# Kernel optimization log

Measured on AMD Instinct MI355X. Metric: run time of the kernel, lower is better.

## Reference

```python
import jax, jax.numpy as jnp
import numpy as np

B, S = 4, 1024          # 4 prefill sequences of length 1024 (cu_seqlens equal-length)
D_MODEL = 2048
N_HEADS = 32
N_KV_HEADS = 8
HEAD_DIM = D_MODEL // N_HEADS          # 64
GROUPS = N_HEADS // N_KV_HEADS         # 4
ROPE_THETA = 10000.0
SCALE = HEAD_DIM ** -0.5


def setup_inputs() -> dict:
    key = jax.random.key(0)
    ks = jax.random.split(key, 6)
    T = B * S
    hidden_states = jax.random.normal(ks[0], (T, D_MODEL), jnp.float32)
    # rotary tables: positions restart per sequence (prefill)
    pos = jnp.tile(jnp.arange(S, dtype=jnp.float32), B)            # [T]
    inv_freq = 1.0 / (ROPE_THETA ** (jnp.arange(0, HEAD_DIM, 2, dtype=jnp.float32) / HEAD_DIM))
    freqs = pos[:, None] * inv_freq[None, :]                        # [T, HEAD_DIM/2]
    cos, sin = jnp.cos(freqs), jnp.sin(freqs)
    std = D_MODEL ** -0.5
    Wq = jax.random.normal(ks[1], (D_MODEL, N_HEADS * HEAD_DIM), jnp.float32) * std
    Wk = jax.random.normal(ks[2], (D_MODEL, N_KV_HEADS * HEAD_DIM), jnp.float32) * std
    Wv = jax.random.normal(ks[3], (D_MODEL, N_KV_HEADS * HEAD_DIM), jnp.float32) * std
    Wo = jax.random.normal(ks[4], (N_HEADS * HEAD_DIM, D_MODEL), jnp.float32) * std
    return {"hidden_states": hidden_states, "cos": cos, "sin": sin,
            "Wq": Wq, "Wk": Wk, "Wv": Wv, "Wo": Wo}


def _rope(x, cos, sin):
    # NeoX-style rotary: x [T, H, D], cos/sin [T, D/2]
    half = x.shape[-1] // 2
    x1, x2 = x[..., :half], x[..., half:]
    c, s = cos[:, None, :], sin[:, None, :]
    return jnp.concatenate([x1 * c - x2 * s, x2 * c + x1 * s], axis=-1)


def reference(hidden_states, cos, sin, Wq, Wk, Wv, Wo):
    T = hidden_states.shape[0]
    q = (hidden_states @ Wq).reshape(T, N_HEADS, HEAD_DIM)
    k = (hidden_states @ Wk).reshape(T, N_KV_HEADS, HEAD_DIM)
    v = (hidden_states @ Wv).reshape(T, N_KV_HEADS, HEAD_DIM)
    q = _rope(q, cos, sin)
    k = _rope(k, cos, sin)
    # equal-length varlen prefill -> [B, S, H, D]
    q = q.reshape(B, S, N_HEADS, HEAD_DIM)
    k = jnp.repeat(k.reshape(B, S, N_KV_HEADS, HEAD_DIM), GROUPS, axis=2)  # GQA expand
    v = jnp.repeat(v.reshape(B, S, N_KV_HEADS, HEAD_DIM), GROUPS, axis=2)
    scores = jnp.einsum("bqhd,bkhd->bhqk", q, k) * SCALE
    causal = jnp.tril(jnp.ones((S, S), dtype=bool))
    scores = jnp.where(causal[None, None], scores, jnp.finfo(scores.dtype).min)
    probs = jax.nn.softmax(scores, axis=-1)
    attn = jnp.einsum("bhqk,bkhd->bqhd", probs, v).reshape(T, N_HEADS * HEAD_DIM)
    return attn @ Wo
```

## Files before the change

### kernel.cpp

```cpp
#include <hip/hip_runtime.h>
#include <type_traits>


typedef __bf16 bf16x8 __attribute__((ext_vector_type(8)));
typedef __bf16 bf16x4 __attribute__((ext_vector_type(4)));
typedef float f32x4 __attribute__((ext_vector_type(4)));
typedef unsigned short u16;
typedef unsigned int u32;

#define DEVI __device__ __forceinline__

DEVI u16 f2bf(float f) {
  u32 u = __builtin_bit_cast(u32, f);
  u += 0x7FFF + ((u >> 16) & 1);
  return (u16)(u >> 16);
}

DEVI void ld16_lds(const void* g, void* l) {
  __builtin_amdgcn_global_load_lds((const __attribute__((address_space(1))) u32*)g,
                                   (__attribute__((address_space(3))) u32*)l, 16, 0, 0);
}

__global__ __launch_bounds__(256) void convert_f32_bf16(const float* __restrict__ src,
                                                        u16* __restrict__ dst, int n4) {
  int i = blockIdx.x * 256 + threadIdx.x;
  if (i >= n4) return;
  float4 v = ((const float4*)src)[i];
  ushort4 o;
  o.x = f2bf(v.x); o.y = f2bf(v.y); o.z = f2bf(v.z); o.w = f2bf(v.w);
  ((ushort4*)dst)[i] = o;
}

__global__ __launch_bounds__(256) void trans_f32_bf16(const float* __restrict__ src,
                                                      u16* __restrict__ dst, int R, int C,
                                                      float scale) {
  __shared__ float tile[32][33];
  int c0 = blockIdx.x * 32, r0 = blockIdx.y * 32;
  int tx = threadIdx.x & 31, ty = threadIdx.x >> 5;
#pragma unroll
  for (int i = 0; i < 32; i += 8)
    tile[ty + i][tx] = src[(size_t)(r0 + ty + i) * C + (c0 + tx)];
  __syncthreads();
#pragma unroll
  for (int i = 0; i < 32; i += 8)
    dst[(size_t)(c0 + ty + i) * R + (r0 + tx)] = f2bf(tile[tx][ty + i] * scale);
}

template <typename OutT, bool ROPE>
__global__ __launch_bounds__(256) void gemm_bt(const u16* __restrict__ A, const u16* __restrict__ BT,
                                               OutT* __restrict__ C, int M, int N, int K,
                                               const float* __restrict__ cs,
                                               const float* __restrict__ sn) {
  __shared__ u16 As[128 * 64];
  __shared__ u16 Bs[128 * 64];
  const int tid = threadIdx.x;
  const int lane = tid & 63, wave = tid >> 6;
  const int quad = lane >> 4, l16 = lane & 15;
  const int m0 = blockIdx.y * 128, n0 = blockIdx.x * 128;
  const int wr = (wave >> 1) * 64, wc = (wave & 1) * 64;

  f32x4 acc[4][4] = {};

  const int srow = tid >> 3;
  const int sc = (tid & 7) ^ (srow & 7);
  const u16* Ag = A + (size_t)(m0 + srow) * K + sc * 8;
  const u16* Bg = BT + (size_t)(n0 + srow) * K + sc * 8;

  for (int k0 = 0; k0 < K; k0 += 64) {
    __syncthreads();
#pragma unroll
    for (int i = 0; i < 4; i++) {
      ld16_lds(Ag + k0 + (size_t)i * 32 * K, &As[tid * 8 + i * 2048]);
      ld16_lds(Bg + k0 + (size_t)i * 32 * K, &Bs[tid * 8 + i * 2048]);
    }
    __syncthreads();

#pragma unroll
    for (int s = 0; s < 2; s++) {
      bf16x8 af[4], bfr[4];
#pragma unroll
      for (int i = 0; i < 4; i++) {
        int ar = wr + i * 16 + l16;
        af[i] = *(const bf16x8*)&As[ar * 64 + (((s * 4 + quad) ^ (ar & 7)) * 8)];
        int br = wc + i * 16 + l16;
        bfr[i] = *(const bf16x8*)&Bs[br * 64 + (((s * 4 + quad) ^ (br & 7)) * 8)];
      }
#pragma unroll
      for (int i = 0; i < 4; i++)
#pragma unroll
        for (int j = 0; j < 4; j++)
          acc[i][j] = __builtin_amdgcn_mfma_f32_16x16x32_bf16(af[i], bfr[j], acc[i][j], 0, 0, 0);
    }
  }

  if constexpr (ROPE) {
    if (n0 + wc < 2560) {
#pragma unroll
      for (int i = 0; i < 4; i++) {
        int t0 = m0 + wr + i * 16 + quad * 4;
#pragma unroll
        for (int jj = 0; jj < 2; jj++) {
          int d = jj * 16 + l16;
#pragma unroll
          for (int r = 0; r < 4; r++) {
            float c = cs[(size_t)(t0 + r) * 32 + d];
            float s = sn[(size_t)(t0 + r) * 32 + d];
            float x1 = acc[i][jj][r], x2 = acc[i][jj + 2][r];
            acc[i][jj][r] = x1 * c - x2 * s;
            acc[i][jj + 2][r] = x2 * c + x1 * s;
          }
        }
      }
    }
  }

#pragma unroll
  for (int i = 0; i < 4; i++) {
    int row = m0 + wr + i * 16 + quad * 4;
#pragma unroll
    for (int j = 0; j < 4; j++) {
      int col = n0 + wc + j * 16 + l16;
#pragma unroll
      for (int r = 0; r < 4; r++) {
        size_t off = (size_t)(row + r) * N + col;
        if constexpr (sizeof(OutT) == 2) C[off] = f2bf(acc[i][j][r]);
        else C[off] = acc[i][j][r];
      }
    }
  }
}

__global__ __launch_bounds__(256) void vkt_build(const u16* __restrict__ qkv,
                                                 u16* __restrict__ vkt) {
  __shared__ u16 Vn[128 * 64];
  const int kt = blockIdx.x, kvh = blockIdx.y, b = blockIdx.z;
  const int tid = threadIdx.x;
  const u16* src = qkv + ((size_t)b * 1024 + kt * 128) * 3072 + 2560 + kvh * 64;
  {
    int tok = tid >> 1, hf = tid & 1;
    const uint4* s4 = (const uint4*)(src + (size_t)tok * 3072 + hf * 32);
    uint4* d4 = (uint4*)&Vn[tok * 64 + hf * 32];
#pragma unroll
    for (int j = 0; j < 4; j++) d4[j] = s4[j];
  }
  __syncthreads();
  u16* img = vkt + ((((size_t)b * 8 + kvh) * 8 + kt) << 13);
#pragma unroll
  for (int i = 0; i < 4; i++) {
    int c = tid * 4 + i;
    int dd = c >> 4, chsw = c & 15;
    int ch = chsw ^ (dd & 15);
    u16 tmp[8];
#pragma unroll
    for (int p = 0; p < 8; p++) {
      int col = ch * 8 + p;
      int g = col >> 5, kl = col & 31;
      int kph = ((kl >> 2) & 1) * 16 + ((kl >> 4) & 1) * 8 + ((kl >> 3) & 1) * 4 + (kl & 3);
      tmp[p] = Vn[(g * 32 + kph) * 64 + dd];
    }
    *(uint4*)&img[c * 8] = *(const uint4*)tmp;
  }
}

__global__ __launch_bounds__(256, 2) void flash_attn(const u16* __restrict__ qkv,
                                                     const u16* __restrict__ vkt,
                                                     u16* __restrict__ attn) {
  __shared__ u16 Ks[2][128 * 64];
  __shared__ u16 VT[2][64 * 128];

  const int tid = threadIdx.x;
  const int lane = tid & 63, wave = tid >> 6;
  const int quad = lane >> 4, l16 = lane & 15;
  const int qtA = blockIdx.x, qtB = 7 - blockIdx.x;
  const int h = blockIdx.y, b = blockIdx.z, kvh = h >> 2;
  const size_t tokBase = (size_t)b * 1024;
  const int qcol = h * 64, kcol = 2048 + kvh * 64;
  const int srow = tid >> 3, spc = tid & 7, ssc = spc ^ (srow & 7);

  auto stageK = [&](const u16* gbase, u16* L) {
#pragma unroll
    for (int i = 0; i < 4; i++)
      ld16_lds(gbase + (size_t)(srow + i * 32) * 3072 + ssc * 8, &L[tid * 8 + i * 2048]);
  };
  const u16* vimg = vkt + (((size_t)b * 8 + kvh) << 16);
  auto stageV = [&](int kt, u16* L) {
    const u16* g = vimg + ((size_t)kt << 13);
#pragma unroll
    for (int i = 0; i < 4; i++)
      ld16_lds(g + i * 2048 + tid * 8, &L[tid * 8 + i * 2048]);
  };

  stageK(qkv + (tokBase + qtA * 128) * 3072 + qcol, Ks[0]);
  stageK(qkv + (tokBase + qtB * 128) * 3072 + qcol, Ks[1]);
  __syncthreads();
  bf16x8 qfA[2][2], qfB[2][2];
#pragma unroll
  for (int nq = 0; nq < 2; nq++) {
    int qrow = wave * 32 + nq * 16 + l16;
#pragma unroll
    for (int ks = 0; ks < 2; ks++) {
      int c = (ks * 4 + quad) ^ (qrow & 7);
      qfA[nq][ks] = *(const bf16x8*)&Ks[0][qrow * 64 + c * 8];
      qfB[nq][ks] = *(const bf16x8*)&Ks[1][qrow * 64 + c * 8];
    }
  }
  __syncthreads();

  float lA[2] = {0.f, 0.f}, lB[2] = {0.f, 0.f};
  f32x4 oA[4][2] = {}, oB[4][2] = {};

  auto proc = [&](const bf16x8 (&kf)[2][2], const bf16x8 (&va)[4], const bf16x8 (&qf)[2][2],
                  f32x4 (&o)[4][2], float (&lacc)[2], bool msk, int c) {
    f32x4 s[2][2] = {};
#pragma unroll
    for (int mkl = 0; mkl < 2; mkl++)
#pragma unroll
      for (int ks = 0; ks < 2; ks++) {
        s[0][mkl] = __builtin_amdgcn_mfma_f32_16x16x32_bf16(kf[mkl][ks], qf[0][ks], s[0][mkl], 0, 0, 0);
        s[1][mkl] = __builtin_amdgcn_mfma_f32_16x16x32_bf16(kf[mkl][ks], qf[1][ks], s[1][mkl], 0, 0, 0);
      }
    if (msk) {
#pragma unroll
      for (int nq = 0; nq < 2; nq++) {
        int q = wave * 32 + nq * 16 + l16;
#pragma unroll
        for (int mkl = 0; mkl < 2; mkl++)
#pragma unroll
          for (int r = 0; r < 4; r++)
            if ((c * 2 + mkl) * 16 + quad * 4 + r > q) s[nq][mkl][r] = -3e38f;
      }
    }
    bf16x8 pf[2];
#pragma unroll
    for (int nq = 0; nq < 2; nq++) {
      float a0 = 0.f;
#pragma unroll
      for (int mkl = 0; mkl < 2; mkl++)
#pragma unroll
        for (int r = 0; r < 4; r++) {
          float p = __builtin_amdgcn_exp2f(s[nq][mkl][r]);
          s[nq][mkl][r] = p;
          a0 += p;
        }
      lacc[nq] += a0;
      pf[nq][0] = (__bf16)s[nq][0][0]; pf[nq][1] = (__bf16)s[nq][0][1];
      pf[nq][2] = (__bf16)s[nq][0][2]; pf[nq][3] = (__bf16)s[nq][0][3];
      pf[nq][4] = (__bf16)s[nq][1][0]; pf[nq][5] = (__bf16)s[nq][1][1];
      pf[nq][6] = (__bf16)s[nq][1][2]; pf[nq][7] = (__bf16)s[nq][1][3];
    }
#pragma unroll
    for (int md = 0; md < 4; md++) {
      o[md][0] = __builtin_amdgcn_mfma_f32_16x16x32_bf16(va[md], pf[0], o[md][0], 0, 0, 0);
      o[md][1] = __builtin_amdgcn_mfma_f32_16x16x32_bf16(va[md], pf[1], o[md][1], 0, 0, 0);
    }
  };

  stageK(qkv + tokBase * 3072 + kcol, Ks[0]);
  stageV(0, VT[0]);

  for (int kt = 0; kt <= qtB; kt++) {
    const int cur = kt & 1;
    __syncthreads();
    if (kt < qtB) {
      stageK(qkv + (tokBase + (kt + 1) * 128) * 3072 + kcol, Ks[1 - cur]);
      stageV(kt + 1, VT[1 - cur]);
    }
    const bool doA = (kt <= qtA), mA = (kt == qtA), mB = (kt == qtB);
    const u16* K = Ks[cur];
    const u16* V = VT[cur];
#pragma unroll
    for (int c = 0; c < 4; c++) {
      bf16x8 kf[2][2];
#pragma unroll
      for (int mkl = 0; mkl < 2; mkl++) {
        int krow = (c * 2 + mkl) * 16 + l16;
#pragma unroll
        for (int ks = 0; ks < 2; ks++)
          kf[mkl][ks] = *(const bf16x8*)&K[krow * 64 + ((ks * 4 + quad) ^ (krow & 7)) * 8];
      }
      bf16x8 va[4];
#pragma unroll
      for (int md = 0; md < 4; md++) {
        int dd = md * 16 + l16;
        va[md] = *(const bf16x8*)&V[dd * 128 + ((c * 4 + quad) ^ l16) * 8];
      }
      proc(kf, va, qfB, oB, lB, mB, c);
      if (doA) proc(kf, va, qfA, oA, lA, mA, c);
    }
  }

  auto epilogue = [&](const f32x4 (&o)[4][2], const float (&lacc)[2], int qt_tile) {
#pragma unroll
    for (int nq = 0; nq < 2; nq++) {
      float l = lacc[nq];
      l += __shfl_xor(l, 16);
      l += __shfl_xor(l, 32);
      float inv = 1.0f / l;
      int t = qt_tile * 128 + wave * 32 + nq * 16 + l16;
      size_t rowOff = (tokBase + t) * 2048 + qcol;
#pragma unroll
      for (int md = 0; md < 4; md++) {
        bf16x4 w;
        w[0] = (__bf16)(o[md][nq][0] * inv);
        w[1] = (__bf16)(o[md][nq][1] * inv);
        w[2] = (__bf16)(o[md][nq][2] * inv);
        w[3] = (__bf16)(o[md][nq][3] * inv);
        *(bf16x4*)&attn[rowOff + md * 16 + quad * 4] = w;
      }
    }
  };
  epilogue(oB, lB, qtB);
  epilogue(oA, lA, qtA);
}

extern "C" void kernel_launch(void* const* d_in, const int* in_sizes, int n_in,
                              void* d_out, int out_size, void* d_ws, size_t ws_size,
                              hipStream_t stream) {
  const float* hs = (const float*)d_in[0];
  const float* cs = (const float*)d_in[1];
  const float* sn = (const float*)d_in[2];
  const float* Wq = (const float*)d_in[3];
  const float* Wk = (const float*)d_in[4];
  const float* Wv = (const float*)d_in[5];
  const float* Wo = (const float*)d_in[6];
  float* out = (float*)d_out;

  char* ws = (char*)d_ws;
  u16* hsB   = (u16*)(ws);
  u16* vkt   = (u16*)(ws);
  u16* wqkvT = (u16*)(ws + 16777216);
  u16* woT   = (u16*)(ws + 29360128);
  u16* qkv   = (u16*)(ws + 37748736);
  u16* attnB = (u16*)(ws + 62914560);

  const float QSCALE = 0.18033688011112042f;

  convert_f32_bf16<<<8192, 256, 0, stream>>>(hs, hsB, 4096 * 2048 / 4);
  trans_f32_bf16<<<dim3(64, 64), 256, 0, stream>>>(Wq, wqkvT, 2048, 2048, QSCALE);
  trans_f32_bf16<<<dim3(16, 64), 256, 0, stream>>>(Wk, wqkvT + (size_t)2048 * 2048, 2048, 512, 1.0f);
  trans_f32_bf16<<<dim3(16, 64), 256, 0, stream>>>(Wv, wqkvT + (size_t)2560 * 2048, 2048, 512, 1.0f);
  trans_f32_bf16<<<dim3(64, 64), 256, 0, stream>>>(Wo, woT, 2048, 2048, 1.0f);

  gemm_bt<u16, true><<<dim3(24, 32), 256, 0, stream>>>(hsB, wqkvT, qkv, 4096, 3072, 2048, cs, sn);
  vkt_build<<<dim3(8, 8, 4), 256, 0, stream>>>(qkv, vkt);
  flash_attn<<<dim3(4, 32, 4), 256, 0, stream>>>(qkv, vkt, attnB);
  gemm_bt<float, false><<<dim3(16, 32), 256, 0, stream>>>(attnB, woT, out, 4096, 2048, 2048,
                                                          nullptr, nullptr);
}
```

Measured before the change: 281.1 us.

## Merge prep kernels into one launch and halve GEMM K-tile to 32

The five conversion and transpose launches become a single prep kernel that dispatches work by block index, which removes per-launch overhead and idle gaps between kernels. Separately, the GEMM K-step drops from 64 to 32, halving LDS use per block. A new swizzled layout packs two rows per 64-element LDS line, aiming for higher occupancy. The smaller K-step doubles the number of barrier pairs per output tile and cuts the MFMA work between syncs.

```diff
diff --git a/kernel.cpp b/kernel.cpp
--- a/kernel.cpp
+++ b/kernel.cpp
@@ -21,21 +21,33 @@
                                    (__attribute__((address_space(3))) u32*)l, 16, 0, 0);
 }
 
-__global__ __launch_bounds__(256) void convert_f32_bf16(const float* __restrict__ src,
-                                                        u16* __restrict__ dst, int n4) {
-  int i = blockIdx.x * 256 + threadIdx.x;
-  if (i >= n4) return;
-  float4 v = ((const float4*)src)[i];
-  ushort4 o;
-  o.x = f2bf(v.x); o.y = f2bf(v.y); o.z = f2bf(v.z); o.w = f2bf(v.w);
-  ((ushort4*)dst)[i] = o;
-}
-
-__global__ __launch_bounds__(256) void trans_f32_bf16(const float* __restrict__ src,
-                                                      u16* __restrict__ dst, int R, int C,
-                                                      float scale) {
+__global__ __launch_bounds__(256) void prep(const float* __restrict__ hs, u16* __restrict__ hsB,
+                                            const float* __restrict__ Wq, const float* __restrict__ Wk,
+                                            const float* __restrict__ Wv, const float* __restrict__ Wo,
+                                            u16* __restrict__ wqkvT, u16* __restrict__ woT,
+                                            float qscale) {
+  int bx = blockIdx.x;
+  if (bx < 8192) {
+    int i = bx * 256 + threadIdx.x;
+    float4 v = ((const float4*)hs)[i];
+    ushort4 o;
+    o.x = f2bf(v.x); o.y = f2bf(v.y); o.z = f2bf(v.z); o.w = f2bf(v.w);
+    ((ushort4*)hsB)[i] = o;
+    return;
+  }
+  bx -= 8192;
+  const float* src; u16* dst; int C; float scale; int bxx, bxy;
+  if (bx < 4096)      { src = Wq; dst = wqkvT;                      C = 2048; scale = qscale;
+                        bxx = bx & 63; bxy = bx >> 6; }
+  else if (bx < 5120) { bx -= 4096; src = Wk; dst = wqkvT + (size_t)2048 * 2048; C = 512; scale = 1.f;
+                        bxx = bx & 15; bxy = bx >> 4; }
+  else if (bx < 6144) { bx -= 5120; src = Wv; dst = wqkvT + (size_t)2560 * 2048; C = 512; scale = 1.f;
+                        bxx = bx & 15; bxy = bx >> 4; }
+  else                { bx -= 6144; src = Wo; dst = woT;            C = 2048; scale = 1.f;
+                        bxx = bx & 63; bxy = bx >> 6; }
+  const int R = 2048;
   __shared__ float tile[32][33];
-  int c0 = blockIdx.x * 32, r0 = blockIdx.y * 32;
+  int c0 = bxx * 32, r0 = bxy * 32;
   int tx = threadIdx.x & 31, ty = threadIdx.x >> 5;
 #pragma unroll
   for (int i = 0; i < 32; i += 8)
@@ -51,8 +63,8 @@
                                                OutT* __restrict__ C, int M, int N, int K,
                                                const float* __restrict__ cs,
                                                const float* __restrict__ sn) {
-  __shared__ u16 As[128 * 64];
-  __shared__ u16 Bs[128 * 64];
+  __shared__ u16 As[64 * 64];
+  __shared__ u16 Bs[64 * 64];
   const int tid = threadIdx.x;
   const int lane = tid & 63, wave = tid >> 6;
   const int quad = lane >> 4, l16 = lane & 15;
@@ -61,36 +73,35 @@
 
   f32x4 acc[4][4] = {};
 
-  const int srow = tid >> 3;
-  const int sc = (tid & 7) ^ (srow & 7);
-  const u16* Ag = A + (size_t)(m0 + srow) * K + sc * 8;
-  const u16* Bg = BT + (size_t)(n0 + srow) * K + sc * 8;
-
-  for (int k0 = 0; k0 < K; k0 += 64) {
+  const int s_local = tid >> 3;
+  const int pos = tid & 7;
+  const int v = pos ^ (s_local & 7);
+  const int base_r = 2 * s_local + (v >> 2);
+  const int c0 = v & 3;
+  const u16* Ag = A + (size_t)(m0 + base_r) * K + c0 * 8;
+  const u16* Bg = BT + (size_t)(n0 + base_r) * K + c0 * 8;
+
+  for (int k0 = 0; k0 < K; k0 += 32) {
     __syncthreads();
+    ld16_lds(Ag + k0, &As[tid * 8]);
+    ld16_lds(Ag + k0 + (size_t)64 * K, &As[tid * 8 + 2048]);
+    ld16_lds(Bg + k0, &Bs[tid * 8]);
+    ld16_lds(Bg + k0 + (size_t)64 * K, &Bs[tid * 8 + 2048]);
+    __syncthreads();
+
+    bf16x8 af[4], bfr[4];
 #pragma unroll
     for (int i = 0; i < 4; i++) {
-      ld16_lds(Ag + k0 + (size_t)i * 32 * K, &As[tid * 8 + i * 2048]);
-      ld16_lds(Bg + k0 + (size_t)i * 32 * K, &Bs[tid * 8 + i * 2048]);
-    }
-    __syncthreads();
-
-#pragma unroll
-    for (int s = 0; s < 2; s++) {
-      bf16x8 af[4], bfr[4];
-#pragma unroll
-      for (int i = 0; i < 4; i++) {
-        int ar = wr + i * 16 + l16;
-        af[i] = *(const bf16x8*)&As[ar * 64 + (((s * 4 + quad) ^ (ar & 7)) * 8)];
-        int br = wc + i * 16 + l16;
-        bfr[i] = *(const bf16x8*)&Bs[br * 64 + (((s * 4 + quad) ^ (br & 7)) * 8)];
-      }
-#pragma unroll
-      for (int i = 0; i < 4; i++)
-#pragma unroll
-        for (int j = 0; j < 4; j++)
-          acc[i][j] = __builtin_amdgcn_mfma_f32_16x16x32_bf16(af[i], bfr[j], acc[i][j], 0, 0, 0);
-    }
+      int ar = wr + i * 16 + l16;
+      af[i] = *(const bf16x8*)&As[(ar >> 1) * 64 + ((((ar & 1) * 4 + quad) ^ ((ar >> 1) & 7)) * 8)];
+      int br = wc + i * 16 + l16;
+      bfr[i] = *(const bf16x8*)&Bs[(br >> 1) * 64 + ((((br & 1) * 4 + quad) ^ ((br >> 1) & 7)) * 8)];
+    }
+#pragma unroll
+    for (int i = 0; i < 4; i++)
+#pragma unroll
+      for (int j = 0; j < 4; j++)
+        acc[i][j] = __builtin_amdgcn_mfma_f32_16x16x32_bf16(af[i], bfr[j], acc[i][j], 0, 0, 0);
   }
 
   if constexpr (ROPE) {
@@ -335,12 +346,7 @@
 
   const float QSCALE = 0.18033688011112042f;
 
-  convert_f32_bf16<<<8192, 256, 0, stream>>>(hs, hsB, 4096 * 2048 / 4);
-  trans_f32_bf16<<<dim3(64, 64), 256, 0, stream>>>(Wq, wqkvT, 2048, 2048, QSCALE);
-  trans_f32_bf16<<<dim3(16, 64), 256, 0, stream>>>(Wk, wqkvT + (size_t)2048 * 2048, 2048, 512, 1.0f);
-  trans_f32_bf16<<<dim3(16, 64), 256, 0, stream>>>(Wv, wqkvT + (size_t)2560 * 2048, 2048, 512, 1.0f);
-  trans_f32_bf16<<<dim3(64, 64), 256, 0, stream>>>(Wo, woT, 2048, 2048, 1.0f);
-
+  prep<<<18432, 256, 0, stream>>>(hs, hsB, Wq, Wk, Wv, Wo, wqkvT, woT, QSCALE);
   gemm_bt<u16, true><<<dim3(24, 32), 256, 0, stream>>>(hsB, wqkvT, qkv, 4096, 3072, 2048, cs, sn);
   vkt_build<<<dim3(8, 8, 4), 256, 0, stream>>>(qkv, vkt);
   flash_attn<<<dim3(4, 32, 4), 256, 0, stream>>>(qkv, vkt, attnB);
```

Result: slower. 311.2 us (+10.7%).
